# Kernel tuning notes

Measured on AMD Instinct MI355X. Metric: run time of the kernel, lower is better.

## Reference

```python
import jax, jax.numpy as jnp
import numpy as np

B, N, K = 8, 2048, 20  # clouds, points per cloud, knn


def _lin(k, i, o):
    kw, kb = jax.random.split(k)
    w = jax.random.normal(kw, (i, o), jnp.float32) / np.sqrt(i)
    b = jax.random.normal(kb, (o,), jnp.float32) * 0.01
    return w, b


def setup_inputs():
    key = jax.random.key(0)
    ks = jax.random.split(key, 9)
    pos = jax.random.normal(ks[0], (B * N, 3), jnp.float32)
    w11, b11 = _lin(ks[1], 3, 64)
    w12, b12 = _lin(ks[2], 64, 64)
    w13, b13 = _lin(ks[3], 64, 64)
    w21, b21 = _lin(ks[4], 192, 128)
    wh1, bh1 = _lin(ks[5], 128, 1024)
    wh2, bh2 = _lin(ks[6], 1024, 512)
    wh3, bh3 = _lin(ks[7], 512, 265)
    wh4, bh4 = _lin(ks[8], 265, 40)
    o, z = jnp.ones, jnp.zeros
    return dict(
        pos=pos,
        w11=w11, b11=b11, g11=o(64), be11=z(64),
        w12=w12, b12=b12, g12=o(64), be12=z(64),
        w13=w13, b13=b13, g13=o(64), be13=z(64),
        w21=w21, b21=b21, g21=o(128), be21=z(128),
        wh1=wh1, bh1=bh1, gh1=o(1024), beh1=z(1024),
        wh2=wh2, bh2=bh2, gh2=o(512), beh2=z(512),
        wh3=wh3, bh3=bh3, gh3=o(265), beh3=z(265),
        wh4=wh4, bh4=bh4,
    )


def _bn(x, g, b):
    # BatchNorm1d in training mode: stats over all leading dims, biased var.
    ax = tuple(range(x.ndim - 1))
    m = x.mean(ax)
    v = x.var(ax)
    return (x - m) * jax.lax.rsqrt(v + 1e-5) * g + b


def _forward(pos, w11, b11, g11, be11, w12, b12, g12, be12, w13, b13, g13, be13,
             w21, b21, g21, be21, wh1, bh1, gh1, beh1, wh2, bh2, gh2, beh2,
             wh3, bh3, gh3, beh3, wh4, bh4):
    p = pos.reshape(B, N, 3)
    # knn_graph per cloud, loop=False
    d2 = jnp.sum(p * p, -1)                                   # [B,N]
    dist = d2[:, :, None] + d2[:, None, :] - 2.0 * jnp.einsum('bnd,bmd->bnm', p, p)
    dist = dist + jnp.eye(N, dtype=pos.dtype) * 1e10          # exclude self
    _, idx = jax.lax.top_k(-dist, K)                          # [B,N,K]
    nb = jax.vmap(lambda a, i: a[i])(p, idx)                  # [B,N,K,3]
    rel = nb - p[:, :, None, :]                               # relative neighbor offsets
    # local PCA frame per point (V_t)
    cov = jnp.einsum('bnkd,bnke->bnde', rel, rel)             # [B,N,3,3]
    _, V = jnp.linalg.eigh(cov)                               # columns = principal dirs
    loc = jnp.einsum('bnkd,bnde->bnke', rel, V)               # rel pos in local frame
    # DD1: edge MLP (conv_p) + directional max pool (out_3d)
    h = _bn(jax.nn.relu(loc @ w11 + b11), g11, be11)
    h = _bn(jax.nn.relu(h @ w12 + b12), g12, be12)
    h = _bn(jax.nn.relu(h @ w13 + b13), g13, be13)            # [B,N,K,64]
    f3d = jnp.max(h[..., None] * loc[..., None, :], axis=2)   # [B,N,64,3]
    # DD2: gather neighbor 3d features (conv_fn), rotate into center frame, MLP, max pool
    fj = jax.vmap(lambda a, i: a[i])(f3d, idx)                # [B,N,K,64,3]
    fj_loc = jnp.einsum('bnkcd,bnde->bnkce', fj, V)
    h2 = _bn(jax.nn.relu(fj_loc.reshape(B, N, K, 192) @ w21 + b21), g21, be21)
    fdd2 = jnp.max(h2, axis=2).reshape(B * N, 128)
    # head
    y1 = (fdd2 @ wh1 + bh1).reshape(B, N, 1024).max(axis=1)
    y1 = _bn(jax.nn.relu(y1), gh1, beh1)
    y2 = _bn(jax.nn.relu(y1 @ wh2 + bh2), gh2, beh2)
    y3 = _bn(jax.nn.relu(y2 @ wh3 + bh3), gh3, beh3)
    return jax.nn.log_softmax(y3 @ wh4 + bh4, axis=1)         # [B,40]


def reference(pos, w11, b11, g11, be11, w12, b12, g12, be12, w13, b13, g13, be13,
              w21, b21, g21, be21, wh1, bh1, gh1, beh1, wh2, bh2, gh2, beh2,
              wh3, bh3, gh3, beh3, wh4, bh4):
    return _forward(pos, w11, b11, g11, be11, w12, b12, g12, be12, w13, b13, g13, be13,
                    w21, b21, g21, be21, wh1, bh1, gh1, beh1, wh2, bh2, gh2, beh2,
                    wh3, bh3, gh3, beh3, wh4, bh4)
```

## Files before the change

### kernel.cpp

```cpp
#include <hip/hip_runtime.h>


#define NEW_SLARTG 1

typedef unsigned short u16;
typedef unsigned int u32;
typedef unsigned long long u64;
typedef __attribute__((ext_vector_type(8))) short short8;
typedef __attribute__((ext_vector_type(4))) float f32x4;

#define BB 8
#define NNp 2048
#define KKn 20
#define NP 16384
#define EE 327680

__device__ __forceinline__ u32 fkey(float f) {
  u32 u = __float_as_uint(f);
  return (u & 0x80000000u) ? ~u : (u | 0x80000000u);
}
__device__ __forceinline__ float funkey(u32 k) {
  u32 u = (k & 0x80000000u) ? (k ^ 0x80000000u) : ~k;
  return __uint_as_float(u);
}
__device__ __forceinline__ float f_sign(float a, float b) {
  return (b >= 0.f) ? fabsf(a) : -fabsf(a);
}
__device__ __forceinline__ u16 f2bf(float f) {
  u32 u = __float_as_uint(f);
  u32 r = (u + 0x7fffu + ((u >> 16) & 1u)) >> 16;
  return (u16)r;
}

__device__ __forceinline__ u64 sxor64(u64 v, int m) {
  union { u64 q; u32 d[2]; } a; a.q = v;
  a.d[0] = __shfl_xor(a.d[0], m);
  a.d[1] = __shfl_xor(a.d[1], m);
  return a.q;
}
__device__ __forceinline__ u64 sidx64(u64 v, int src) {
  union { u64 q; u32 d[2]; } a; a.q = v;
  a.d[0] = __shfl(a.d[0], src);
  a.d[1] = __shfl(a.d[1], src);
  return a.q;
}
__device__ __forceinline__ void bsort64(u64& v, int lane) {
#pragma unroll
  for (int k = 2; k <= 64; k <<= 1) {
#pragma unroll
    for (int j = k >> 1; j > 0; j >>= 1) {
      u64 pv = sxor64(v, j);
      bool up = ((lane & k) == 0);
      bool lower = ((lane & j) == 0);
      bool keepmin = (lower == up);
      bool take = keepmin ? (pv < v) : (pv > v);
      v = take ? pv : v;
    }
  }
}

__device__ float slapy2_(float x, float y) {
#pragma clang fp contract(off)
  float xa = fabsf(x), ya = fabsf(y);
  float w = fmaxf(xa, ya), z = fminf(xa, ya);
  if (z == 0.f) return w;
  float t = z / w;
  return w * sqrtf(1.0f + t * t);
}

__device__ void slartg_(float f, float g, float& c, float& s, float& r) {
#pragma clang fp contract(off)
#if NEW_SLARTG
  const float safmin = 1.17549435e-38f;
  const float safmax = 8.50705917e+37f;
  const float rtmin = 1.08420217e-19f;
  const float rtmax = 6.52221171e+18f;
  float f1 = fabsf(f), g1 = fabsf(g);
  if (g == 0.f) { c = 1.f; s = 0.f; r = f; }
  else if (f == 0.f) { c = 0.f; s = (g >= 0.f) ? 1.f : -1.f; r = g1; }
  else {
    float d;
    if (f1 > rtmin && f1 < rtmax && g1 > rtmin && g1 < rtmax) {
      d = sqrtf(f * f + g * g);
      c = f1 / d;
      r = (f >= 0.f) ? d : -d;
    } else {
      float uu = fminf(safmax, fmaxf(safmin, fmaxf(f1, g1)));
      float fs = f / uu, gs = g / uu;
      d = sqrtf(fs * fs + gs * gs);
      c = fabsf(fs) / d;
      r = ((f >= 0.f) ? d : -d) * uu;
    }
    s = g / r;
  }
#else
  if (g == 0.f) { c = 1.f; s = 0.f; r = f; }
  else if (f == 0.f) { c = 0.f; s = 1.f; r = g; }
  else {
    float f1 = f, g1 = g;
    r = sqrtf(f1 * f1 + g1 * g1);
    c = f1 / r;
    s = g1 / r;
    if (fabsf(f) > fabsf(g) && c < 0.f) { c = -c; s = -s; r = -r; }
  }
#endif
}

__device__ void slaev2_(float a, float b, float c, float& rt1, float& rt2,
                        float& cs1, float& sn1) {
#pragma clang fp contract(off)
  float sm = a + c;
  float df = a - c;
  float adf = fabsf(df);
  float tb = b + b;
  float ab = fabsf(tb);
  float acmx, acmn;
  if (fabsf(a) > fabsf(c)) { acmx = a; acmn = c; } else { acmx = c; acmn = a; }
  float rt;
  if (adf > ab) { float t = ab / adf; rt = adf * sqrtf(1.f + t * t); }
  else if (adf < ab) { float t = adf / ab; rt = ab * sqrtf(1.f + t * t); }
  else { rt = ab * sqrtf(2.f); }
  int sgn1;
  if (sm < 0.f) {
    rt1 = 0.5f * (sm - rt); sgn1 = -1;
    rt2 = (acmx / rt1) * acmn - (b / rt1) * b;
  } else if (sm > 0.f) {
    rt1 = 0.5f * (sm + rt); sgn1 = 1;
    rt2 = (acmx / rt1) * acmn - (b / rt1) * b;
  } else {
    rt1 = 0.5f * rt; rt2 = -0.5f * rt; sgn1 = 1;
  }
  float cs; int sgn2;
  if (df >= 0.f) { cs = df + rt; sgn2 = 1; } else { cs = df - rt; sgn2 = -1; }
  float acs = fabsf(cs);
  if (acs > ab) {
    float ct = -tb / cs;
    sn1 = 1.f / sqrtf(1.f + ct * ct);
    cs1 = ct * sn1;
  } else {
    if (ab == 0.f) { cs1 = 1.f; sn1 = 0.f; }
    else {
      float tn = -cs / tb;
      cs1 = 1.f / sqrtf(1.f + tn * tn);
      sn1 = tn * cs1;
    }
  }
  if (sgn1 == sgn2) { float tn = cs1; cs1 = -sn1; sn1 = tn; }
}

__device__ void ssteqr3_(float* d, float* e, float z[3][3]) {
#pragma clang fp contract(off)
  const float eps = 5.9604645e-08f;
  const float eps2 = 3.5527137e-15f;
  const float safmin = 1.17549435e-38f;
  const int n = 3;
  const int nmaxit = 90;
  int jtot = 0;
  int l1 = 1;

  while (1) {
    if (l1 > n) break;
    if (l1 > 1) e[l1 - 2] = 0.f;
    int m = n;
    if (l1 <= n - 1) {
      for (int mm = l1; mm <= n - 1; ++mm) {
        float tst = fabsf(e[mm - 1]);
        if (tst == 0.f) { m = mm; break; }
        if (tst <= (sqrtf(fabsf(d[mm - 1])) * sqrtf(fabsf(d[mm]))) * eps) {
          e[mm - 1] = 0.f; m = mm; break;
        }
      }
    }
    int l = l1, lsv = l, lend = m, lendsv = lend;
    (void)lsv; (void)lendsv;
    l1 = m + 1;
    if (lend == l) continue;

    float anorm = 0.f;
    for (int i = l; i <= lend; ++i) anorm = fmaxf(anorm, fabsf(d[i - 1]));
    for (int i = l; i <= lend - 1; ++i) anorm = fmaxf(anorm, fabsf(e[i - 1]));
    if (anorm == 0.f) continue;

    if (fabsf(d[lend - 1]) < fabsf(d[l - 1])) { lend = lsv; l = lendsv; }

    if (lend > l) {
      while (1) {
        int m2 = lend;
        if (l != lend) {
          for (int mm = l; mm <= lend - 1; ++mm) {
            float tst = fabsf(e[mm - 1]); tst = tst * tst;
            if (tst <= (eps2 * fabsf(d[mm - 1])) * fabsf(d[mm]) + safmin) { m2 = mm; break; }
          }
        }
        if (m2 < lend) e[m2 - 1] = 0.f;
        float p = d[l - 1];
        if (m2 == l) {
          d[l - 1] = p; l += 1;
          if (l <= lend) continue;
          break;
        }
        if (m2 == l + 1) {
          float rt1, rt2, cc, ss;
          slaev2_(d[l - 1], e[l - 1], d[l], rt1, rt2, cc, ss);
          for (int i = 0; i < 3; ++i) {
            float temp = z[i][l];
            z[i][l] = cc * temp - ss * z[i][l - 1];
            z[i][l - 1] = ss * temp + cc * z[i][l - 1];
          }
          d[l - 1] = rt1; d[l] = rt2; e[l - 1] = 0.f;
          l += 2;
          if (l <= lend) continue;
          break;
        }
        if (jtot == nmaxit) break;
        jtot++;
        float g = (d[l] - p) / (2.f * e[l - 1]);
        float r = slapy2_(g, 1.f);
        g = d[m2 - 1] - p + (e[l - 1] / (g + f_sign(r, g)));
        float s = 1.f, c = 1.f;
        p = 0.f;
        float csv[2], snv[2];
        for (int i = m2 - 1; i >= l; --i) {
          float f = s * e[i - 1];
          float b = c * e[i - 1];
          slartg_(g, f, c, s, r);
          if (i != m2 - 1) e[i] = r;
          g = d[i] - p;
          r = (d[i - 1] - g) * s + (2.f * c) * b;
          p = s * r;
          d[i] = g + p;
          g = c * r - b;
          csv[i - l] = c; snv[i - l] = -s;
        }
        int cnt = m2 - l;
        for (int j = cnt; j >= 1; --j) {
          float cj = csv[j - 1], sj = snv[j - 1];
          int c0 = (l - 1) + (j - 1);
          for (int i = 0; i < 3; ++i) {
            float temp = z[i][c0 + 1];
            z[i][c0 + 1] = cj * temp - sj * z[i][c0];
            z[i][c0] = sj * temp + cj * z[i][c0];
          }
        }
        d[l - 1] = d[l - 1] - p;
        e[l - 1] = g;
      }
    } else {
      while (1) {
        int m2 = lend;
        if (l != lend) {
          for (int mm = l; mm >= lend + 1; --mm) {
            float tst = fabsf(e[mm - 2]); tst = tst * tst;
            if (tst <= (eps2 * fabsf(d[mm - 1])) * fabsf(d[mm - 2]) + safmin) { m2 = mm; break; }
          }
        }
        if (m2 > lend) e[m2 - 2] = 0.f;
        float p = d[l - 1];
        if (m2 == l) {
          d[l - 1] = p; l -= 1;
          if (l >= lend) continue;
          break;
        }
        if (m2 == l - 1) {
          float rt1, rt2, cc, ss;
          slaev2_(d[l - 2], e[l - 2], d[l - 1], rt1, rt2, cc, ss);
          for (int i = 0; i < 3; ++i) {
            float temp = z[i][l - 1];
            z[i][l - 1] = cc * temp - ss * z[i][l - 2];
            z[i][l - 2] = ss * temp + cc * z[i][l - 2];
          }
          d[l - 2] = rt1; d[l - 1] = rt2; e[l - 2] = 0.f;
          l -= 2;
          if (l >= lend) continue;
          break;
        }
        if (jtot == nmaxit) break;
        jtot++;
        float g = (d[l - 2] - p) / (2.f * e[l - 2]);
        float r = slapy2_(g, 1.f);
        g = d[m2 - 1] - p + (e[l - 2] / (g + f_sign(r, g)));
        float s = 1.f, c = 1.f;
        p = 0.f;
        float csv[2], snv[2];
        for (int i = m2; i <= l - 1; ++i) {
          float f = s * e[i - 1];
          float b = c * e[i - 1];
          slartg_(g, f, c, s, r);
          if (i != m2) e[i - 2] = r;
          g = d[i - 1] - p;
          r = (d[i] - g) * s + (2.f * c) * b;
          p = s * r;
          d[i - 1] = g + p;
          g = c * r - b;
          csv[i - m2] = c; snv[i - m2] = s;
        }
        int cnt = l - m2;
        for (int j = 1; j <= cnt; ++j) {
          float cj = csv[j - 1], sj = snv[j - 1];
          int c0 = (m2 - 1) + (j - 1);
          for (int i = 0; i < 3; ++i) {
            float temp = z[i][c0 + 1];
            z[i][c0 + 1] = cj * temp - sj * z[i][c0];
            z[i][c0] = sj * temp + cj * z[i][c0];
          }
        }
        d[l - 1] = d[l - 1] - p;
        e[l - 2] = g;
      }
    }
  }

  for (int ii = 2; ii <= n; ++ii) {
    int i = ii - 1, k = i;
    float p = d[i - 1];
    for (int j = ii; j <= n; ++j)
      if (d[j - 1] < p) { k = j; p = d[j - 1]; }
    if (k != i) {
      d[k - 1] = d[i - 1]; d[i - 1] = p;
      for (int r2 = 0; r2 < 3; ++r2) {
        float t = z[r2][i - 1]; z[r2][i - 1] = z[r2][k - 1]; z[r2][k - 1] = t;
      }
    }
  }
}

__device__ void eigh3_(float a00, float a10, float a11, float a20, float a21,
                       float a22, float V[3][3]) {
#pragma clang fp contract(off)
  float d0, d1, d2, e0, e1, tau1 = 0.f, v2 = 0.f;
  {
    float alpha = a10;
    float xnorm = fabsf(a20);
    if (xnorm == 0.f) {
      tau1 = 0.f; v2 = 0.f;
      e0 = alpha; d0 = a00; d1 = a11; d2 = a22; e1 = a21;
    } else {
      float beta = -f_sign(slapy2_(alpha, xnorm), alpha);
      tau1 = (beta - alpha) / beta;
      float inv = 1.0f / (alpha - beta);
      v2 = a20 * inv;
      float y0 = tau1 * a11;
      float y1v = tau1 * a21;
      float temp2 = a21 * v2;
      y0 = y0 + tau1 * temp2;
      y1v = y1v + (tau1 * v2) * a22;
      float dotyv = y0 * 1.f + y1v * v2;
      float al = (-0.5f * tau1) * dotyv;
      float w0 = y0 + al * 1.f;
      float w1 = y1v + al * v2;
      a11 = (a11 + 1.f * (-w0)) + w0 * (-1.f);
      a21 = (a21 + v2 * (-w0)) + w1 * (-1.f);
      a22 = (a22 + v2 * (-w1)) + w1 * (-v2);
      e0 = beta; d0 = a00; d1 = a11; d2 = a22; e1 = a21;
    }
  }
  float dd[3] = { d0, d1, d2 };
  float ee[2] = { e0, e1 };
  float z[3][3] = { {1.f,0.f,0.f},{0.f,1.f,0.f},{0.f,0.f,1.f} };
  ssteqr3_(dd, ee, z);
  if (tau1 != 0.f) {
    for (int j = 0; j < 3; ++j) {
      float wj = z[1][j] * 1.f + z[2][j] * v2;
      float temp = -tau1 * wj;
      z[1][j] = z[1][j] + 1.f * temp;
      z[2][j] = z[2][j] + v2 * temp;
    }
  }
  for (int r = 0; r < 3; ++r)
    for (int cix = 0; cix < 3; ++cix)
      V[r][cix] = z[r][cix];
}


__global__ void zero_kernel(double* sb, int nd, u32* p2, int n2) {
  int t = blockIdx.x * blockDim.x + threadIdx.x;
  if (t < nd) sb[t] = 0.0;
  if (t < n2) p2[t] = 0u;
}

__global__ __launch_bounds__(256) void knn_kernel(const float* __restrict__ pos,
                                                  int* __restrict__ idx) {
#pragma clang fp contract(off)
  __shared__ u64 cke[4][128];
  int w = threadIdx.x >> 6;
  int lane = threadIdx.x & 63;
  int wid = blockIdx.x * 4 + w;
  int b = wid >> 11;
  int n = wid & 2047;
  const float* pc = pos + (size_t)b * NNp * 3;
  float qx = pc[n * 3 + 0], qy = pc[n * 3 + 1], qz = pc[n * 3 + 2];
  float d2n = (qx * qx + qy * qy) + qz * qz;

  u32 kreg[32];
  u32 mk = 0xFFFFFFFFu;
#pragma unroll
  for (int t = 0; t < 32; ++t) {
    int m = lane + 64 * t;
    float x = pc[m * 3 + 0], y = pc[m * 3 + 1], zc = pc[m * 3 + 2];
    float d2m = (x * x + y * y) + zc * zc;
    float dot = (qx * x + qy * y) + qz * zc;
    float dist = (d2n + d2m) - 2.0f * dot;
    u32 key = fkey(dist);
    if (m == n) key = 0xFFFFFFFFu;
    kreg[t] = key;
    mk = key < mk ? key : mk;
  }
#pragma unroll
  for (int off = 32; off; off >>= 1) {
    u32 o = __shfl_xor(mk, off);
    mk = o < mk ? o : mk;
  }

  u32 lo_b = mk - 1u, hi_b = 0xFFFFFFFEu;
  int c_hi = 2047;
  float tf = funkey(mk) * 7.368f;
  u32 T = fkey(tf);
  if (T < mk) T = mk;
  if (T > 0xFFFFFFFEu) T = 0xFFFFFFFEu;
  for (int it = 0; it < 48; ++it) {
    int cnt = 0;
#pragma unroll
    for (int t = 0; t < 32; ++t) cnt += (kreg[t] <= T) ? 1 : 0;
#pragma unroll
    for (int off = 32; off; off >>= 1) cnt += __shfl_xor(cnt, off);
    if (cnt >= 20) {
      hi_b = T; c_hi = cnt;
      if (cnt <= 128) break;
    } else {
      lo_b = T;
    }
    if (hi_b <= lo_b + 1u) break;
    u32 Tn;
    if (it < 12) {
      float tfc = funkey(T);
      int cc = cnt < 1 ? 1 : cnt;
      float guess = tfc * __builtin_exp2f(0.66667f * __builtin_log2f(45.0f / (float)cc));
      Tn = fkey(guess);
      if (!(Tn > lo_b && Tn < hi_b)) Tn = lo_b + ((hi_b - lo_b) >> 1);
    } else {
      Tn = lo_b + ((hi_b - lo_b) >> 1);
    }
    T = Tn;
  }

  u64* ck = cke[w];
  u32 base = 0;
#pragma unroll
  for (int t = 0; t < 32; ++t) {
    bool pass = kreg[t] <= hi_b;
    u64 ball = __ballot(pass);
    if (pass) {
      u32 posn = base + (u32)__popcll(ball & ((1ull << lane) - 1ull));
      if (posn < 128u)
        ck[posn] = ((u64)kreg[t] << 32) | (u32)(lane + 64 * t);
    }
    base += (u32)__popcll(ball);
  }
  if (base > 128u) {
    base = 0;
#pragma unroll
    for (int t = 0; t < 32; ++t) {
      bool pass = kreg[t] <= lo_b;
      u64 ball = __ballot(pass);
      if (pass) {
        u32 posn = base + (u32)__popcll(ball & ((1ull << lane) - 1ull));
        ck[posn] = ((u64)kreg[t] << 32) | (u32)(lane + 64 * t);
      }
      base += (u32)__popcll(ball);
    }
#pragma unroll
    for (int t = 0; t < 32; ++t) {
      bool pass = (kreg[t] > lo_b) && (kreg[t] <= hi_b);
      u64 ball = __ballot(pass);
      if (pass) {
        u32 posn = base + (u32)__popcll(ball & ((1ull << lane) - 1ull));
        if (posn < 128u)
          ck[posn] = ((u64)kreg[t] << 32) | (u32)(lane + 64 * t);
      }
      base += (u32)__popcll(ball);
    }
  }
  u32 ctot = base < 128u ? base : 128u;

  u64 e0 = (lane < (int)ctot) ? ck[lane] : ~0ull;
  bsort64(e0, lane);
  if (ctot > 64u) {
    u64 e1 = (lane + 64 < (int)ctot) ? ck[lane + 64] : ~0ull;
    bsort64(e1, lane);
    u64 r = sidx64(e1, 63 - lane);
    u64 mn = r < e0 ? r : e0;
#pragma unroll
    for (int j = 32; j > 0; j >>= 1) {
      u64 pv = sxor64(mn, j);
      bool lower2 = ((lane & j) == 0);
      bool take = lower2 ? (pv < mn) : (pv > mn);
      mn = take ? pv : mn;
    }
    e0 = mn;
  }
  if (lane < 20)
    idx[(size_t)wid * 20 + lane] = (int)(u32)(e0 & 0xFFFFFFFFull);
}

__global__ __launch_bounds__(64) void prep_kernel(const float* __restrict__ pos,
                                                  const int* __restrict__ idx,
                                                  float* __restrict__ loc,
                                                  float* __restrict__ Vout) {
#pragma clang fp contract(off)
  int p = blockIdx.x * 64 + threadIdx.x;
  int b = p >> 11, n = p & 2047;
  const float* pc = pos + (size_t)b * NNp * 3;
  float qx = pc[n * 3 + 0], qy = pc[n * 3 + 1], qz = pc[n * 3 + 2];
  const int* ip = idx + (size_t)p * 20;
  float c00 = 0, c01 = 0, c02 = 0, c11 = 0, c12 = 0, c22 = 0;
  for (int k = 0; k < 20; ++k) {
    int j = ip[k];
    float rx = pc[j * 3 + 0] - qx, ry = pc[j * 3 + 1] - qy, rz = pc[j * 3 + 2] - qz;
    c00 += rx * rx; c01 += rx * ry; c02 += rx * rz;
    c11 += ry * ry; c12 += ry * rz; c22 += rz * rz;
  }
  float Vm[3][3];
  eigh3_(c00, c01, c11, c02, c12, c22, Vm);
  float* vp = Vout + (size_t)p * 9;
  for (int d = 0; d < 3; ++d)
    for (int e = 0; e < 3; ++e) vp[d * 3 + e] = Vm[d][e];
  for (int k = 0; k < 20; ++k) {
    int j = ip[k];
    float rx = pc[j * 3 + 0] - qx, ry = pc[j * 3 + 1] - qy, rz = pc[j * 3 + 2] - qz;
    float l0 = rx * Vm[0][0] + ry * Vm[1][0] + rz * Vm[2][0];
    float l1 = rx * Vm[0][1] + ry * Vm[1][1] + rz * Vm[2][1];
    float l2 = rx * Vm[0][2] + ry * Vm[1][2] + rz * Vm[2][2];
    size_t e = ((size_t)p * 20 + k) * 3;
    loc[e + 0] = l0; loc[e + 1] = l1; loc[e + 2] = l2;
  }
}

__global__ __launch_bounds__(256) void l1_kernel(const float* __restrict__ loc,
                                                 const float* __restrict__ W,
                                                 const float* __restrict__ bias,
                                                 float* __restrict__ h1,
                                                 double* __restrict__ sb) {
  __shared__ float sW[192];
  __shared__ float sB[64];
  __shared__ float red[512];
  int t = threadIdx.x;
  if (t < 192) sW[t] = W[t];
  if (t < 64) sB[t] = bias[t];
  __syncthreads();
  int w = t >> 6, c = t & 63;
  size_t e0 = (size_t)blockIdx.x * 256 + w * 64;
  float wc0 = sW[c], wc1 = sW[64 + c], wc2 = sW[128 + c], bc = sB[c];
  float s = 0.f, q = 0.f;
  for (int e = 0; e < 64; ++e) {
    float x0 = loc[(e0 + e) * 3 + 0];
    float x1 = loc[(e0 + e) * 3 + 1];
    float x2 = loc[(e0 + e) * 3 + 2];
    float z = fmaxf(bc + x0 * wc0 + x1 * wc1 + x2 * wc2, 0.f);
    h1[(e0 + e) * 64 + c] = z;
    s += z; q += z * z;
  }
  red[w * 64 + c] = s;
  red[256 + w * 64 + c] = q;
  __syncthreads();
  if (t < 64) {
    float S = red[t] + red[64 + t] + red[128 + t] + red[192 + t];
    float Q = red[256 + t] + red[320 + t] + red[384 + t] + red[448 + t];
    atomicAdd(&sb[((int)blockIdx.x & 63) * 128 + t], (double)S);
    atomicAdd(&sb[((int)blockIdx.x & 63) * 128 + 64 + t], (double)Q);
  }
}

__global__ void finalizeB_kernel(const double* __restrict__ sb,
                                 const float* __restrict__ g,
                                 const float* __restrict__ be,
                                 float* __restrict__ outp) {
  int c = threadIdx.x;
  if (c >= 64) return;
  double s = 0.0, q = 0.0;
  for (int buk = 0; buk < 64; ++buk) {
    s += sb[buk * 128 + c];
    q += sb[buk * 128 + 64 + c];
  }
  double m = s / (double)EE;
  double var = q / (double)EE - m * m;
  double inv = 1.0 / sqrt(var + 1e-5);
  double sc = (double)g[c] * inv;
  outp[c] = (float)sc;
  outp[64 + c] = (float)((double)be[c] - m * sc);
}

__global__ void finalize64_kernel(const double* __restrict__ s4b,
                                  const float* __restrict__ g,
                                  const float* __restrict__ be,
                                  float* __restrict__ outp) {
  int c = threadIdx.x;
  double s = 0.0, q = 0.0;
  for (int buk = 0; buk < 64; ++buk) {
    s += s4b[buk * 256 + c];
    q += s4b[buk * 256 + 128 + c];
  }
  double m = s / (double)EE;
  double var = q / (double)EE - m * m;
  double inv = 1.0 / sqrt(var + 1e-5);
  double sc = (double)g[c] * inv;
  outp[c] = (float)sc;
  outp[128 + c] = (float)((double)be[c] - m * sc);
}

__global__ __launch_bounds__(256) void wsplit_kernel(const float* __restrict__ w12,
                                                     const float* __restrict__ w13,
                                                     u16* __restrict__ wsp) {
  int id = blockIdx.x * 256 + threadIdx.x;
  if (id >= 8192) return;
  int layer = id >> 12;
  int nk = id & 4095;
  int n = nk >> 6, k = nk & 63;
  const float* W = layer ? w13 : w12;
  float v = W[(size_t)k * 64 + n];
  u16 hi = f2bf(v);
  float rem = v - __uint_as_float(((u32)hi) << 16);
  u16 lo = f2bf(rem);
  wsp[layer * 8192 + n * 64 + k] = hi;
  wsp[layer * 8192 + 4096 + n * 64 + k] = lo;
}

__global__ __launch_bounds__(256) void l23_kernel(const float* __restrict__ hin,
                                                  const float* __restrict__ ss,
                                                  const u16* __restrict__ whi,
                                                  const u16* __restrict__ wlo,
                                                  const float* __restrict__ bias,
                                                  float* __restrict__ hout,
                                                  double* __restrict__ sb) {
  __shared__ u16 sHI[128 * 72];
  __shared__ u16 sLO[128 * 72];
  int t = threadIdx.x;
  size_t e0 = (size_t)blockIdx.x * 128;
  int w = t >> 6, l = t & 63;
  int lr = l & 15, lg = l >> 4;

  short8 bhi[4][2], blo[4][2];
#pragma unroll
  for (int nt = 0; nt < 4; ++nt)
#pragma unroll
    for (int ks = 0; ks < 2; ++ks) {
      int off = (nt * 16 + lr) * 64 + ks * 32 + lg * 8;
      bhi[nt][ks] = *(const short8*)&whi[off];
      blo[nt][ks] = *(const short8*)&wlo[off];
    }

  for (int v = t; v < 128 * 16; v += 256) {
    int el = v >> 4, cq = v & 15;
    float4 x4 = *(const float4*)&hin[(e0 + el) * 64 + cq * 4];
    float4 sc4 = *(const float4*)&ss[cq * 4];
    float4 sh4 = *(const float4*)&ss[64 + cq * 4];
    float vv[4];
    vv[0] = x4.x * sc4.x + sh4.x;
    vv[1] = x4.y * sc4.y + sh4.y;
    vv[2] = x4.z * sc4.z + sh4.z;
    vv[3] = x4.w * sc4.w + sh4.w;
    u16 hi[4], lo[4];
#pragma unroll
    for (int j = 0; j < 4; ++j) {
      hi[j] = f2bf(vv[j]);
      float rem = vv[j] - __uint_as_float(((u32)hi[j]) << 16);
      lo[j] = f2bf(rem);
    }
    u32* ph = (u32*)&sHI[el * 72 + cq * 4];
    ph[0] = (u32)hi[0] | ((u32)hi[1] << 16);
    ph[1] = (u32)hi[2] | ((u32)hi[3] << 16);
    u32* pl = (u32*)&sLO[el * 72 + cq * 4];
    pl[0] = (u32)lo[0] | ((u32)lo[1] << 16);
    pl[1] = (u32)lo[2] | ((u32)lo[3] << 16);
  }
  __syncthreads();

  f32x4 acc[2][4];
#pragma unroll
  for (int mt = 0; mt < 2; ++mt)
#pragma unroll
    for (int nt = 0; nt < 4; ++nt) acc[mt][nt] = (f32x4)(0.f);

#pragma unroll
  for (int ks = 0; ks < 2; ++ks) {
    const int kb = ks * 32 + lg * 8;
#pragma unroll
    for (int mt = 0; mt < 2; ++mt) {
      int row = w * 32 + mt * 16 + lr;
      short8 ah = *(const short8*)&sHI[row * 72 + kb];
      short8 al = *(const short8*)&sLO[row * 72 + kb];
#pragma unroll
      for (int nt = 0; nt < 4; ++nt) {
        acc[mt][nt] = __builtin_amdgcn_mfma_f32_16x16x32_bf16(ah, bhi[nt][ks], acc[mt][nt], 0, 0, 0);
        acc[mt][nt] = __builtin_amdgcn_mfma_f32_16x16x32_bf16(al, bhi[nt][ks], acc[mt][nt], 0, 0, 0);
        acc[mt][nt] = __builtin_amdgcn_mfma_f32_16x16x32_bf16(ah, blo[nt][ks], acc[mt][nt], 0, 0, 0);
      }
    }
  }

#pragma unroll
  for (int nt = 0; nt < 4; ++nt) {
    int o = nt * 16 + lr;
    float bs = bias[o];
    float s = 0.f, q = 0.f;
#pragma unroll
    for (int mt = 0; mt < 2; ++mt) {
#pragma unroll
      for (int r = 0; r < 4; ++r) {
        float z = fmaxf(acc[mt][nt][r] + bs, 0.f);
        size_t e = e0 + w * 32 + mt * 16 + lg * 4 + r;
        hout[e * 64 + o] = z;
        s += z; q += z * z;
      }
    }
    s += __shfl_xor(s, 16); s += __shfl_xor(s, 32);
    q += __shfl_xor(q, 16); q += __shfl_xor(q, 32);
    if (l < 16) {
      atomicAdd(&sb[((int)blockIdx.x & 63) * 128 + o], (double)s);
      atomicAdd(&sb[((int)blockIdx.x & 63) * 128 + 64 + o], (double)q);
    }
  }
}

__global__ __launch_bounds__(256) void f3d_kernel(const float* __restrict__ h3,
                                                  const float* __restrict__ ss3,
                                                  const float* __restrict__ loc,
                                                  float* __restrict__ f3d) {
  int t = threadIdx.x;
  int p = blockIdx.x * 4 + (t >> 6);
  int c = t & 63;
  float sc = ss3[c], sh = ss3[64 + c];
  float m0 = -__builtin_inff(), m1 = m0, m2 = m0;
  size_t eb = (size_t)p * 20;
  for (int k = 0; k < 20; ++k) {
    size_t e = eb + k;
    float h = h3[e * 64 + c] * sc + sh;
    float l0 = loc[e * 3 + 0], l1 = loc[e * 3 + 1], l2 = loc[e * 3 + 2];
    m0 = fmaxf(m0, h * l0);
    m1 = fmaxf(m1, h * l1);
    m2 = fmaxf(m2, h * l2);
  }
  size_t o = (size_t)p * 192 + c * 3;
  f3d[o + 0] = m0; f3d[o + 1] = m1; f3d[o + 2] = m2;
}

__global__ __launch_bounds__(256) void wtcvt_kernel(const float* __restrict__ W,
                                                    u16* __restrict__ wt,
                                                    double* __restrict__ s4b) {
  int id = blockIdx.x * 256 + threadIdx.x;
  if (id < 192 * 128) {
    int n = id / 192, k = id - n * 192;
    wt[id] = f2bf(W[(size_t)k * 128 + n]);
  }
  if (id < 64 * 256) s4b[id] = 0.0;
}

__global__ __launch_bounds__(256) void dd2_kernel(const float* __restrict__ f3d,
                                                  const float* __restrict__ Vmat,
                                                  const int* __restrict__ idx,
                                                  const u16* __restrict__ wt,
                                                  const float* __restrict__ bias,
                                                  float* __restrict__ fdd2T,
                                                  double* __restrict__ s4b) {
  __shared__ u16 sX[80 * 200];
  __shared__ float sV[36];
  __shared__ int sJ[80];
  int t = threadIdx.x;
  int wk = (blockIdx.x & 7) * 512 + (blockIdx.x >> 3);
  int p0 = wk * 4;
  int bcl = p0 >> 11;
  int buk = ((int)blockIdx.x & 63) << 8;

  int w = t >> 6, l = t & 63;
  int lr = l & 15, lg = l >> 4;

  short8 breg[2][6];
#pragma unroll
  for (int nt = 0; nt < 2; ++nt)
#pragma unroll
    for (int s = 0; s < 6; ++s) {
      const int kk = (s / 3) * 96 + (s % 3) * 32 + lg * 8;
      breg[nt][s] = *(const short8*)&wt[(w * 32 + nt * 16 + lr) * 192 + kk];
    }

  if (t < 36) sV[t] = Vmat[(size_t)p0 * 9 + t];
  if (t < 80) sJ[t] = ((bcl << 11) + idx[(size_t)p0 * 20 + t]) * 192;
  __syncthreads();

  for (int v = t; v < 80 * 32; v += 256) {
    int el = v >> 5, c2 = v & 31;
    int pp = el / 20;
    const float* fp = f3d + (size_t)sJ[el] + 6 * c2;
    float f0 = fp[0], f1 = fp[1], f2 = fp[2];
    float f3 = fp[3], f4 = fp[4], f5 = fp[5];
    const float* Vp = &sV[pp * 9];
    float x0 = f0 * Vp[0] + f1 * Vp[3] + f2 * Vp[6];
    float x1 = f0 * Vp[1] + f1 * Vp[4] + f2 * Vp[7];
    float x2 = f0 * Vp[2] + f1 * Vp[5] + f2 * Vp[8];
    float y0 = f3 * Vp[0] + f4 * Vp[3] + f5 * Vp[6];
    float y1 = f3 * Vp[1] + f4 * Vp[4] + f5 * Vp[7];
    float y2 = f3 * Vp[2] + f4 * Vp[5] + f5 * Vp[8];
    u32* xp = (u32*)&sX[el * 200 + 6 * c2];
    xp[0] = (u32)f2bf(x0) | ((u32)f2bf(x1) << 16);
    xp[1] = (u32)f2bf(x2) | ((u32)f2bf(y0) << 16);
    xp[2] = (u32)f2bf(y1) | ((u32)f2bf(y2) << 16);
  }
  __syncthreads();

  f32x4 acc[5][2];
#pragma unroll
  for (int mt = 0; mt < 5; ++mt) {
    acc[mt][0] = (f32x4)(0.f);
    acc[mt][1] = (f32x4)(0.f);
  }

#pragma unroll
  for (int s = 0; s < 6; ++s) {
    const int kbase = (s / 3) * 96 + (s % 3) * 32 + lg * 8;
#pragma unroll
    for (int mt = 0; mt < 5; ++mt) {
      short8 a = *(const short8*)&sX[(mt * 16 + lr) * 200 + kbase];
      acc[mt][0] = __builtin_amdgcn_mfma_f32_16x16x32_bf16(a, breg[0][s], acc[mt][0], 0, 0, 0);
      acc[mt][1] = __builtin_amdgcn_mfma_f32_16x16x32_bf16(a, breg[1][s], acc[mt][1], 0, 0, 0);
    }
  }

#pragma unroll
  for (int nt = 0; nt < 2; ++nt) {
    int col = w * 32 + nt * 16 + lr;
    float bs = bias[col];
    float pm0 = 0.f, pm1 = 0.f, pm2 = 0.f, pm3 = 0.f;
    float s = 0.f, q = 0.f;
#pragma unroll
    for (int mt = 0; mt < 5; ++mt) {
#pragma unroll
      for (int r = 0; r < 4; ++r) {
        int edge = mt * 16 + lg * 4 + r;
        float z = fmaxf(acc[mt][nt][r] + bs, 0.f);
        pm0 = fmaxf(pm0, (edge < 20) ? z : 0.f);
        pm1 = fmaxf(pm1, (edge >= 20 && edge < 40) ? z : 0.f);
        pm2 = fmaxf(pm2, (edge >= 40 && edge < 60) ? z : 0.f);
        pm3 = fmaxf(pm3, (edge >= 60) ? z : 0.f);
        s += z; q += z * z;
      }
    }
#pragma unroll
    for (int off = 16; off < 64; off <<= 1) {
      pm0 = fmaxf(pm0, __shfl_xor(pm0, off));
      pm1 = fmaxf(pm1, __shfl_xor(pm1, off));
      pm2 = fmaxf(pm2, __shfl_xor(pm2, off));
      pm3 = fmaxf(pm3, __shfl_xor(pm3, off));
      s += __shfl_xor(s, off);
      q += __shfl_xor(q, off);
    }
    if (l < 16) {
      float4 pv;
      pv.x = pm0; pv.y = pm1; pv.z = pm2; pv.w = pm3;
      *(float4*)&fdd2T[(size_t)col * NP + p0] = pv;
      atomicAdd(&s4b[buk + col], (double)s);
      atomicAdd(&s4b[buk + 128 + col], (double)q);
    }
  }
}

__global__ __launch_bounds__(256) void y1_kernel(const float* __restrict__ fdd2T,
                                                 const float* __restrict__ ss4,
                                                 const float* __restrict__ wh1,
                                                 u32* __restrict__ y1key) {
  __shared__ float sX[64][128];
  __shared__ float sW[64][128];
  int t = threadIdx.x;
  int mtile = blockIdx.x & 127;
  int ntile = blockIdx.x >> 7;
  int cl = mtile >> 4;
  size_t pbase = (size_t)mtile * 128;
  int c0 = ntile * 128;
  int mg = t >> 4, ng = t & 15;

  float acc[8][8];
#pragma unroll
  for (int i = 0; i < 8; ++i)
#pragma unroll
    for (int j = 0; j < 8; ++j) acc[i][j] = 0.f;

  for (int ks = 0; ks < 2; ++ks) {
    int rr = t >> 5, mq = t & 31;
#pragma unroll
    for (int i = 0; i < 8; ++i) {
      int r = rr + i * 8;
      int k = ks * 64 + r;
      float4 x4 = *(const float4*)&fdd2T[(size_t)k * NP + pbase + mq * 4];
      float sc = ss4[k], sh = ss4[128 + k];
      float4 st;
      st.x = x4.x * sc + sh;
      st.y = x4.y * sc + sh;
      st.z = x4.z * sc + sh;
      st.w = x4.w * sc + sh;
      *(float4*)&sX[r][mq * 4] = st;
      float4 w4 = *(const float4*)&wh1[(size_t)k * 1024 + c0 + mq * 4];
      *(float4*)&sW[r][mq * 4] = w4;
    }
    __syncthreads();
#pragma unroll 8
    for (int kk = 0; kk < 64; ++kk) {
      float4 xa = *(const float4*)&sX[kk][mg * 4];
      float4 xb = *(const float4*)&sX[kk][64 + mg * 4];
      float4 wa = *(const float4*)&sW[kk][ng * 4];
      float4 wb = *(const float4*)&sW[kk][64 + ng * 4];
      float xr[8] = { xa.x, xa.y, xa.z, xa.w, xb.x, xb.y, xb.z, xb.w };
      float wc[8] = { wa.x, wa.y, wa.z, wa.w, wb.x, wb.y, wb.z, wb.w };
#pragma unroll
      for (int i = 0; i < 8; ++i)
#pragma unroll
        for (int j = 0; j < 8; ++j) acc[i][j] += xr[i] * wc[j];
    }
    __syncthreads();
  }

  float colmax[8];
#pragma unroll
  for (int j = 0; j < 8; ++j) {
    float v = acc[0][j];
#pragma unroll
    for (int i = 1; i < 8; ++i) v = fmaxf(v, acc[i][j]);
    colmax[j] = v;
  }
  float* red = &sX[0][0];
#pragma unroll
  for (int j = 0; j < 8; ++j) {
    int col = (j < 4) ? (ng * 4 + j) : (64 + ng * 4 + (j - 4));
    red[col * 16 + mg] = colmax[j];
  }
  __syncthreads();
  if (t < 128) {
    float m = red[t * 16];
#pragma unroll
    for (int i = 1; i < 16; ++i) m = fmaxf(m, red[t * 16 + i]);
    atomicMax(&y1key[(size_t)cl * 1024 + c0 + t], fkey(m));
  }
}

__global__ void y1bn_kernel(const u32* __restrict__ y1key,
                            const float* __restrict__ bh1,
                            const float* __restrict__ g,
                            const float* __restrict__ be,
                            float* __restrict__ y1n) {
  int c = blockIdx.x * 256 + threadIdx.x;
  if (c >= 1024) return;
  float bs = bh1[c];
  float v[8]; double s = 0.0;
#pragma unroll
  for (int b = 0; b < 8; ++b) {
    v[b] = fmaxf(funkey(y1key[b * 1024 + c]) + bs, 0.f);
    s += (double)v[b];
  }
  double m = s / 8.0, q = 0.0;
#pragma unroll
  for (int b = 0; b < 8; ++b) { double d = (double)v[b] - m; q += d * d; }
  q /= 8.0;
  double inv = 1.0 / sqrt(q + 1e-5);
  double sg = (double)g[c] * inv;
#pragma unroll
  for (int b = 0; b < 8; ++b)
    y1n[b * 1024 + c] = (float)(((double)v[b] - m) * sg + (double)be[c]);
}

__global__ __launch_bounds__(256) void hgemm_kernel(const float* __restrict__ yin,
                                                    const float* __restrict__ W,
                                                    float* __restrict__ part,
                                                    int INn, int OUTn, int notile) {
  __shared__ float sx[8 * 128];
  __shared__ float red[4][8][64];
  int t = threadIdx.x;
  int og = blockIdx.x % notile;
  int ks = blockIdx.x / notile;
  int KC = INn >> 3;
  int k0 = ks * KC;
  for (int v = t; v < 8 * KC; v += 256) {
    int b = v / KC, i = v - b * KC;
    sx[b * KC + i] = yin[(size_t)b * INn + k0 + i];
  }
  __syncthreads();
  int o = og * 64 + (t & 63);
  int kq = t >> 6;
  int sub = KC >> 2;
  float acc[8];
#pragma unroll
  for (int b = 0; b < 8; ++b) acc[b] = 0.f;
  if (o < OUTn) {
    for (int i = kq * sub; i < kq * sub + sub; ++i) {
      float w = W[(size_t)(k0 + i) * OUTn + o];
#pragma unroll
      for (int b = 0; b < 8; ++b) acc[b] += sx[b * KC + i] * w;
    }
  }
#pragma unroll
  for (int b = 0; b < 8; ++b) red[kq][b][t & 63] = acc[b];
  __syncthreads();
  if (kq == 0 && o < OUTn) {
#pragma unroll
    for (int b = 0; b < 8; ++b) {
      float s = ((red[0][b][t] + red[1][b][t]) + red[2][b][t]) + red[3][b][t];
      part[(size_t)(ks * 8 + b) * 512 + o] = s;
    }
  }
}

__global__ void hreduce_kernel(const float* __restrict__ part,
                               const float* __restrict__ bias,
                               const float* __restrict__ g,
                               const float* __restrict__ be,
                               float* __restrict__ yout, int OUTn) {
  int o = blockIdx.x * 256 + threadIdx.x;
  if (o >= OUTn) return;
  float bs = bias[o];
  float v[8]; double s = 0.0;
#pragma unroll
  for (int b = 0; b < 8; ++b) {
    float p = 0.f;
#pragma unroll
    for (int ks = 0; ks < 8; ++ks) p += part[(size_t)(ks * 8 + b) * 512 + o];
    v[b] = fmaxf(p + bs, 0.f);
    s += (double)v[b];
  }
  double m = s / 8.0, q = 0.0;
#pragma unroll
  for (int b = 0; b < 8; ++b) { double d = (double)v[b] - m; q += d * d; }
  q /= 8.0;
  double inv = 1.0 / sqrt(q + 1e-5);
  double sg = (double)g[o] * inv;
#pragma unroll
  for (int b = 0; b < 8; ++b)
    yout[(size_t)b * OUTn + o] = (float)(((double)v[b] - m) * sg + (double)be[o]);
}

__global__ __launch_bounds__(384) void logits_kernel(const float* __restrict__ y3n,
                                                     const float* __restrict__ W,
                                                     const float* __restrict__ bias,
                                                     float* __restrict__ out) {
  __shared__ float sy[8 * 265];
  __shared__ float slog[320];
  __shared__ float sm[8], sl[8];
  int t = threadIdx.x;
  for (int v = t; v < 8 * 265; v += 384) sy[v] = y3n[v];
  __syncthreads();
  if (t < 320) {
    int b = t / 40, o = t % 40;
    float acc = 0.f;
    for (int i = 0; i < 265; ++i) acc += sy[b * 265 + i] * W[i * 40 + o];
    slog[t] = acc + bias[o];
  }
  __syncthreads();
  if (t < 8) {
    float m = slog[t * 40];
    for (int o = 1; o < 40; ++o) m = fmaxf(m, slog[t * 40 + o]);
    float s = 0.f;
    for (int o = 0; o < 40; ++o) s += expf(slog[t * 40 + o] - m);
    sm[t] = m; sl[t] = logf(s);
  }
  __syncthreads();
  if (t < 320) {
    int b = t / 40;
    out[t] = slog[t] - sm[b] - sl[b];
  }
}

extern "C" void kernel_launch(void* const* d_in, const int* in_sizes, int n_in,
                              void* d_out, int out_size, void* d_ws, size_t ws_size,
                              hipStream_t stream) {
  (void)in_sizes; (void)n_in; (void)out_size; (void)ws_size;
  const float* pos  = (const float*)d_in[0];
  const float* w11  = (const float*)d_in[1];
  const float* b11  = (const float*)d_in[2];
  const float* g11  = (const float*)d_in[3];
  const float* be11 = (const float*)d_in[4];
  const float* w12  = (const float*)d_in[5];
  const float* b12  = (const float*)d_in[6];
  const float* g12  = (const float*)d_in[7];
  const float* be12 = (const float*)d_in[8];
  const float* w13  = (const float*)d_in[9];
  const float* b13  = (const float*)d_in[10];
  const float* g13  = (const float*)d_in[11];
  const float* be13 = (const float*)d_in[12];
  const float* w21  = (const float*)d_in[13];
  const float* b21  = (const float*)d_in[14];
  const float* g21  = (const float*)d_in[15];
  const float* be21 = (const float*)d_in[16];
  const float* wh1  = (const float*)d_in[17];
  const float* bh1  = (const float*)d_in[18];
  const float* gh1  = (const float*)d_in[19];
  const float* beh1 = (const float*)d_in[20];
  const float* wh2  = (const float*)d_in[21];
  const float* bh2  = (const float*)d_in[22];
  const float* gh2  = (const float*)d_in[23];
  const float* beh2 = (const float*)d_in[24];
  const float* wh3  = (const float*)d_in[25];
  const float* bh3  = (const float*)d_in[26];
  const float* gh3  = (const float*)d_in[27];
  const float* beh3 = (const float*)d_in[28];
  const float* wh4  = (const float*)d_in[29];
  const float* bh4  = (const float*)d_in[30];

  char* ws = (char*)d_ws;
  int*    idx   = (int*)(ws + 0);
  float*  loc   = (float*)(ws + 1310720);
  float*  V     = (float*)(ws + 5242880);
  float*  h     = (float*)(ws + 5832704);
  u16*    wt    = (u16*)(ws + 5832704);
  double* s4b   = (double*)(ws + 5898240);
  float*  hpart = (float*)(ws + 6881280);
  float*  f3d   = (float*)(ws + 89718784);
  double* sbkt  = (double*)(ws + 89718784);
  u16*    wsp   = (u16*)(ws + 89718784 + 196608);
  float*  fdd2T = (float*)(ws + 102301696);
  u32*    y1k   = (u32*)(ws + 110690304);
  float*  y1n   = (float*)(ws + 110723072);
  float*  y2n   = (float*)(ws + 110755840);
  float*  y3n   = (float*)(ws + 110772224);
  float*  param = (float*)(ws + 110785856);
  float*  out   = (float*)d_out;

  double* sbL1 = sbkt;
  double* sbL2 = sbkt + 8192;
  double* sbL3 = sbkt + 16384;

  zero_kernel<<<96, 256, 0, stream>>>(sbkt, 24576, y1k, 8192);
  wsplit_kernel<<<32, 256, 0, stream>>>(w12, w13, wsp);
  knn_kernel<<<4096, 256, 0, stream>>>(pos, idx);
  prep_kernel<<<256, 64, 0, stream>>>(pos, idx, loc, V);

  l1_kernel<<<1280, 256, 0, stream>>>(loc, w11, b11, h, sbL1);
  finalizeB_kernel<<<1, 64, 0, stream>>>(sbL1, g11, be11, param);

  l23_kernel<<<2560, 256, 0, stream>>>(h, param, wsp, wsp + 4096, b12, h, sbL2);
  finalizeB_kernel<<<1, 64, 0, stream>>>(sbL2, g12, be12, param + 128);

  l23_kernel<<<2560, 256, 0, stream>>>(h, param + 128, wsp + 8192, wsp + 12288, b13, h, sbL3);
  finalizeB_kernel<<<1, 64, 0, stream>>>(sbL3, g13, be13, param + 256);

  f3d_kernel<<<4096, 256, 0, stream>>>(h, param + 256, loc, f3d);
  wtcvt_kernel<<<96, 256, 0, stream>>>(w21, wt, s4b);
  dd2_kernel<<<4096, 256, 0, stream>>>(f3d, V, idx, wt, b21, fdd2T, s4b);
  finalize64_kernel<<<1, 128, 0, stream>>>(s4b, g21, be21, param + 384);

  y1_kernel<<<1024, 256, 0, stream>>>(fdd2T, param + 384, wh1, y1k);
  y1bn_kernel<<<4, 256, 0, stream>>>(y1k, bh1, gh1, beh1, y1n);

  hgemm_kernel<<<64, 256, 0, stream>>>(y1n, wh2, hpart, 1024, 512, 8);
  hreduce_kernel<<<2, 256, 0, stream>>>(hpart, bh2, gh2, beh2, y2n, 512);
  hgemm_kernel<<<40, 256, 0, stream>>>(y2n, wh3, hpart, 512, 265, 5);
  hreduce_kernel<<<2, 256, 0, stream>>>(hpart, bh3, gh3, beh3, y3n, 265);
  logits_kernel<<<1, 384, 0, stream>>>(y3n, wh4, bh4, out);
}
```

Measured before the change: 370.0 us.

## Fuse head BN/reduce into GEMMs, merge init kernels, tweak dd2 and y1 tiling

Merges the zero and weight-split kernels into one init kernel. The head's BN and partial-sum reduction kernels are folded into the following GEMM and logits kernels, cutting five small launches; each block now recomputes the BN for its slice. dd2 uses float2 gathers and a per-quad max in its epilogue, and y1 halves its shared-memory K tile, which lowers LDS use but doubles the number of sync steps.

```diff
diff --git a/kernel.cpp b/kernel.cpp
--- a/kernel.cpp
+++ b/kernel.cpp
@@ -372,10 +372,26 @@
 }
 
 
-__global__ void zero_kernel(double* sb, int nd, u32* p2, int n2) {
-  int t = blockIdx.x * blockDim.x + threadIdx.x;
-  if (t < nd) sb[t] = 0.0;
-  if (t < n2) p2[t] = 0u;
+__global__ __launch_bounds__(256) void init_kernel(double* __restrict__ sb,
+                                                   u32* __restrict__ y1k,
+                                                   const float* __restrict__ w12,
+                                                   const float* __restrict__ w13,
+                                                   u16* __restrict__ wsp) {
+  int id = blockIdx.x * 256 + threadIdx.x;
+  if (id < 24576) sb[id] = 0.0;
+  if (id < 8192) {
+    y1k[id] = 0u;
+    int layer = id >> 12;
+    int nk = id & 4095;
+    int n = nk >> 6, k = nk & 63;
+    const float* W = layer ? w13 : w12;
+    float v = W[(size_t)k * 64 + n];
+    u16 hi = f2bf(v);
+    float rem = v - __uint_as_float(((u32)hi) << 16);
+    u16 lo = f2bf(rem);
+    wsp[layer * 8192 + n * 64 + k] = hi;
+    wsp[layer * 8192 + 4096 + n * 64 + k] = lo;
+  }
 }
 
 __global__ __launch_bounds__(256) void knn_kernel(const float* __restrict__ pos,
@@ -605,23 +621,6 @@
   double sc = (double)g[c] * inv;
   outp[c] = (float)sc;
   outp[128 + c] = (float)((double)be[c] - m * sc);
-}
-
-__global__ __launch_bounds__(256) void wsplit_kernel(const float* __restrict__ w12,
-                                                     const float* __restrict__ w13,
-                                                     u16* __restrict__ wsp) {
-  int id = blockIdx.x * 256 + threadIdx.x;
-  if (id >= 8192) return;
-  int layer = id >> 12;
-  int nk = id & 4095;
-  int n = nk >> 6, k = nk & 63;
-  const float* W = layer ? w13 : w12;
-  float v = W[(size_t)k * 64 + n];
-  u16 hi = f2bf(v);
-  float rem = v - __uint_as_float(((u32)hi) << 16);
-  u16 lo = f2bf(rem);
-  wsp[layer * 8192 + n * 64 + k] = hi;
-  wsp[layer * 8192 + 4096 + n * 64 + k] = lo;
 }
 
 __global__ __launch_bounds__(256) void l23_kernel(const float* __restrict__ hin,
@@ -790,8 +789,11 @@
     int el = v >> 5, c2 = v & 31;
     int pp = el / 20;
     const float* fp = f3d + (size_t)sJ[el] + 6 * c2;
-    float f0 = fp[0], f1 = fp[1], f2 = fp[2];
-    float f3 = fp[3], f4 = fp[4], f5 = fp[5];
+    float2 f01 = *(const float2*)(fp);
+    float2 f23 = *(const float2*)(fp + 2);
+    float2 f45 = *(const float2*)(fp + 4);
+    float f0 = f01.x, f1 = f01.y, f2 = f23.x;
+    float f3 = f23.y, f4 = f45.x, f5 = f45.y;
     const float* Vp = &sV[pp * 9];
     float x0 = f0 * Vp[0] + f1 * Vp[3] + f2 * Vp[6];
     float x1 = f0 * Vp[1] + f1 * Vp[4] + f2 * Vp[7];
@@ -832,16 +834,21 @@
     float s = 0.f, q = 0.f;
 #pragma unroll
     for (int mt = 0; mt < 5; ++mt) {
-#pragma unroll
-      for (int r = 0; r < 4; ++r) {
-        int edge = mt * 16 + lg * 4 + r;
-        float z = fmaxf(acc[mt][nt][r] + bs, 0.f);
-        pm0 = fmaxf(pm0, (edge < 20) ? z : 0.f);
-        pm1 = fmaxf(pm1, (edge >= 20 && edge < 40) ? z : 0.f);
-        pm2 = fmaxf(pm2, (edge >= 40 && edge < 60) ? z : 0.f);
-        pm3 = fmaxf(pm3, (edge >= 60) ? z : 0.f);
-        s += z; q += z * z;
-      }
+      int qs = mt * 16 + lg * 4;
+      int qp = qs / 20;
+      float z0 = fmaxf(acc[mt][nt][0] + bs, 0.f);
+      float z1 = fmaxf(acc[mt][nt][1] + bs, 0.f);
+      float z2 = fmaxf(acc[mt][nt][2] + bs, 0.f);
+      float z3 = fmaxf(acc[mt][nt][3] + bs, 0.f);
+      s += z0; q += z0 * z0;
+      s += z1; q += z1 * z1;
+      s += z2; q += z2 * z2;
+      s += z3; q += z3 * z3;
+      float qm = fmaxf(fmaxf(z0, z1), fmaxf(z2, z3));
+      pm0 = fmaxf(pm0, (qp == 0) ? qm : 0.f);
+      pm1 = fmaxf(pm1, (qp == 1) ? qm : 0.f);
+      pm2 = fmaxf(pm2, (qp == 2) ? qm : 0.f);
+      pm3 = fmaxf(pm3, (qp == 3) ? qm : 0.f);
     }
 #pragma unroll
     for (int off = 16; off < 64; off <<= 1) {
@@ -866,8 +873,8 @@
                                                  const float* __restrict__ ss4,
                                                  const float* __restrict__ wh1,
                                                  u32* __restrict__ y1key) {
-  __shared__ float sX[64][128];
-  __shared__ float sW[64][128];
+  __shared__ float sX[32][128];
+  __shared__ float sW[32][128];
   int t = threadIdx.x;
   int mtile = blockIdx.x & 127;
   int ntile = blockIdx.x >> 7;
@@ -882,12 +889,12 @@
 #pragma unroll
     for (int j = 0; j < 8; ++j) acc[i][j] = 0.f;
 
-  for (int ks = 0; ks < 2; ++ks) {
+  for (int ks = 0; ks < 4; ++ks) {
     int rr = t >> 5, mq = t & 31;
 #pragma unroll
-    for (int i = 0; i < 8; ++i) {
+    for (int i = 0; i < 4; ++i) {
       int r = rr + i * 8;
-      int k = ks * 64 + r;
+      int k = ks * 32 + r;
       float4 x4 = *(const float4*)&fdd2T[(size_t)k * NP + pbase + mq * 4];
       float sc = ss4[k], sh = ss4[128 + k];
       float4 st;
@@ -901,7 +908,7 @@
     }
     __syncthreads();
 #pragma unroll 8
-    for (int kk = 0; kk < 64; ++kk) {
+    for (int kk = 0; kk < 32; ++kk) {
       float4 xa = *(const float4*)&sX[kk][mg * 4];
       float4 xb = *(const float4*)&sX[kk][64 + mg * 4];
       float4 wa = *(const float4*)&sW[kk][ng * 4];
@@ -939,64 +946,52 @@
   }
 }
 
-__global__ void y1bn_kernel(const u32* __restrict__ y1key,
-                            const float* __restrict__ bh1,
-                            const float* __restrict__ g,
-                            const float* __restrict__ be,
-                            float* __restrict__ y1n) {
-  int c = blockIdx.x * 256 + threadIdx.x;
-  if (c >= 1024) return;
-  float bs = bh1[c];
-  float v[8]; double s = 0.0;
-#pragma unroll
-  for (int b = 0; b < 8; ++b) {
-    v[b] = fmaxf(funkey(y1key[b * 1024 + c]) + bs, 0.f);
-    s += (double)v[b];
-  }
-  double m = s / 8.0, q = 0.0;
-#pragma unroll
-  for (int b = 0; b < 8; ++b) { double d = (double)v[b] - m; q += d * d; }
-  q /= 8.0;
-  double inv = 1.0 / sqrt(q + 1e-5);
-  double sg = (double)g[c] * inv;
-#pragma unroll
-  for (int b = 0; b < 8; ++b)
-    y1n[b * 1024 + c] = (float)(((double)v[b] - m) * sg + (double)be[c]);
-}
-
-__global__ __launch_bounds__(256) void hgemm_kernel(const float* __restrict__ yin,
-                                                    const float* __restrict__ W,
-                                                    float* __restrict__ part,
-                                                    int INn, int OUTn, int notile) {
+__global__ __launch_bounds__(256) void hgemm1_kernel(const u32* __restrict__ y1k,
+                                                     const float* __restrict__ bh1,
+                                                     const float* __restrict__ gh1,
+                                                     const float* __restrict__ beh1,
+                                                     const float* __restrict__ W,
+                                                     float* __restrict__ part) {
   __shared__ float sx[8 * 128];
   __shared__ float red[4][8][64];
   int t = threadIdx.x;
-  int og = blockIdx.x % notile;
-  int ks = blockIdx.x / notile;
-  int KC = INn >> 3;
-  int k0 = ks * KC;
-  for (int v = t; v < 8 * KC; v += 256) {
-    int b = v / KC, i = v - b * KC;
-    sx[b * KC + i] = yin[(size_t)b * INn + k0 + i];
+  int og = blockIdx.x & 7;
+  int ks = blockIdx.x >> 3;
+  int k0 = ks * 128;
+  if (t < 128) {
+    int c = k0 + t;
+    float bs = bh1[c];
+    float v[8]; double s = 0.0;
+#pragma unroll
+    for (int b = 0; b < 8; ++b) {
+      v[b] = fmaxf(funkey(y1k[b * 1024 + c]) + bs, 0.f);
+      s += (double)v[b];
+    }
+    double m = s / 8.0, q = 0.0;
+#pragma unroll
+    for (int b = 0; b < 8; ++b) { double d = (double)v[b] - m; q += d * d; }
+    q /= 8.0;
+    double inv = 1.0 / sqrt(q + 1e-5);
+    double sg = (double)gh1[c] * inv;
+#pragma unroll
+    for (int b = 0; b < 8; ++b)
+      sx[b * 128 + t] = (float)(((double)v[b] - m) * sg + (double)beh1[c]);
   }
   __syncthreads();
   int o = og * 64 + (t & 63);
   int kq = t >> 6;
-  int sub = KC >> 2;
   float acc[8];
 #pragma unroll
   for (int b = 0; b < 8; ++b) acc[b] = 0.f;
-  if (o < OUTn) {
-    for (int i = kq * sub; i < kq * sub + sub; ++i) {
-      float w = W[(size_t)(k0 + i) * OUTn + o];
-#pragma unroll
-      for (int b = 0; b < 8; ++b) acc[b] += sx[b * KC + i] * w;
-    }
+  for (int i = kq * 32; i < kq * 32 + 32; ++i) {
+    float w = W[(size_t)(k0 + i) * 512 + o];
+#pragma unroll
+    for (int b = 0; b < 8; ++b) acc[b] += sx[b * 128 + i] * w;
   }
 #pragma unroll
   for (int b = 0; b < 8; ++b) red[kq][b][t & 63] = acc[b];
   __syncthreads();
-  if (kq == 0 && o < OUTn) {
+  if (kq == 0) {
 #pragma unroll
     for (int b = 0; b < 8; ++b) {
       float s = ((red[0][b][t] + red[1][b][t]) + red[2][b][t]) + red[3][b][t];
@@ -1005,35 +1000,69 @@
   }
 }
 
-__global__ void hreduce_kernel(const float* __restrict__ part,
-                               const float* __restrict__ bias,
-                               const float* __restrict__ g,
-                               const float* __restrict__ be,
-                               float* __restrict__ yout, int OUTn) {
-  int o = blockIdx.x * 256 + threadIdx.x;
-  if (o >= OUTn) return;
-  float bs = bias[o];
-  float v[8]; double s = 0.0;
-#pragma unroll
-  for (int b = 0; b < 8; ++b) {
-    float p = 0.f;
-#pragma unroll
-    for (int ks = 0; ks < 8; ++ks) p += part[(size_t)(ks * 8 + b) * 512 + o];
-    v[b] = fmaxf(p + bs, 0.f);
-    s += (double)v[b];
-  }
-  double m = s / 8.0, q = 0.0;
-#pragma unroll
-  for (int b = 0; b < 8; ++b) { double d = (double)v[b] - m; q += d * d; }
-  q /= 8.0;
-  double inv = 1.0 / sqrt(q + 1e-5);
-  double sg = (double)g[o] * inv;
-#pragma unroll
-  for (int b = 0; b < 8; ++b)
-    yout[(size_t)b * OUTn + o] = (float)(((double)v[b] - m) * sg + (double)be[o]);
-}
-
-__global__ __launch_bounds__(384) void logits_kernel(const float* __restrict__ y3n,
+__global__ __launch_bounds__(256) void hgemm2_kernel(const float* __restrict__ part,
+                                                     const float* __restrict__ bh2,
+                                                     const float* __restrict__ gh2,
+                                                     const float* __restrict__ beh2,
+                                                     const float* __restrict__ W,
+                                                     float* __restrict__ part2) {
+  __shared__ float sx[8 * 64];
+  __shared__ float red[4][8][64];
+  int t = threadIdx.x;
+  int og = blockIdx.x % 5;
+  int ks = blockIdx.x / 5;
+  int k0 = ks * 64;
+  if (t < 64) {
+    int c = k0 + t;
+    float bs = bh2[c];
+    float v[8]; double s = 0.0;
+#pragma unroll
+    for (int b = 0; b < 8; ++b) {
+      float p = 0.f;
+#pragma unroll
+      for (int c2 = 0; c2 < 8; ++c2) p += part[(size_t)(c2 * 8 + b) * 512 + c];
+      v[b] = fmaxf(p + bs, 0.f);
+      s += (double)v[b];
+    }
+    double m = s / 8.0, q = 0.0;
+#pragma unroll
+    for (int b = 0; b < 8; ++b) { double d = (double)v[b] - m; q += d * d; }
+    q /= 8.0;
+    double inv = 1.0 / sqrt(q + 1e-5);
+    double sg = (double)gh2[c] * inv;
+#pragma unroll
+    for (int b = 0; b < 8; ++b)
+      sx[b * 64 + t] = (float)(((double)v[b] - m) * sg + (double)beh2[c]);
+  }
+  __syncthreads();
+  int o = og * 64 + (t & 63);
+  int kq = t >> 6;
+  float acc[8];
+#pragma unroll
+  for (int b = 0; b < 8; ++b) acc[b] = 0.f;
+  if (o < 265) {
+    for (int i = kq * 16; i < kq * 16 + 16; ++i) {
+      float w = W[(size_t)(k0 + i) * 265 + o];
+#pragma unroll
+      for (int b = 0; b < 8; ++b) acc[b] += sx[b * 64 + i] * w;
+    }
+  }
+#pragma unroll
+  for (int b = 0; b < 8; ++b) red[kq][b][t & 63] = acc[b];
+  __syncthreads();
+  if (kq == 0 && o < 265) {
+#pragma unroll
+    for (int b = 0; b < 8; ++b) {
+      float s = ((red[0][b][t] + red[1][b][t]) + red[2][b][t]) + red[3][b][t];
+      part2[(size_t)(ks * 8 + b) * 512 + o] = s;
+    }
+  }
+}
+
+__global__ __launch_bounds__(384) void logits_kernel(const float* __restrict__ part2,
+                                                     const float* __restrict__ bh3,
+                                                     const float* __restrict__ gh3,
+                                                     const float* __restrict__ beh3,
                                                      const float* __restrict__ W,
                                                      const float* __restrict__ bias,
                                                      float* __restrict__ out) {
@@ -1041,7 +1070,27 @@
   __shared__ float slog[320];
   __shared__ float sm[8], sl[8];
   int t = threadIdx.x;
-  for (int v = t; v < 8 * 265; v += 384) sy[v] = y3n[v];
+  if (t < 265) {
+    float bs = bh3[t];
+    float v[8]; double s = 0.0;
+#pragma unroll
+    for (int b = 0; b < 8; ++b) {
+      float p = 0.f;
+#pragma unroll
+      for (int c2 = 0; c2 < 8; ++c2) p += part2[(size_t)(c2 * 8 + b) * 512 + t];
+      v[b] = fmaxf(p + bs, 0.f);
+      s += (double)v[b];
+    }
+    double m = s / 8.0, q = 0.0;
+#pragma unroll
+    for (int b = 0; b < 8; ++b) { double d = (double)v[b] - m; q += d * d; }
+    q /= 8.0;
+    double inv = 1.0 / sqrt(q + 1e-5);
+    double sg = (double)gh3[t] * inv;
+#pragma unroll
+    for (int b = 0; b < 8; ++b)
+      sy[b * 265 + t] = (float)(((double)v[b] - m) * sg + (double)beh3[t]);
+  }
   __syncthreads();
   if (t < 320) {
     int b = t / 40, o = t % 40;
@@ -1108,14 +1157,12 @@
   u16*    wt    = (u16*)(ws + 5832704);
   double* s4b   = (double*)(ws + 5898240);
   float*  hpart = (float*)(ws + 6881280);
+  float*  hpart2= (float*)(ws + 7012352);
   float*  f3d   = (float*)(ws + 89718784);
   double* sbkt  = (double*)(ws + 89718784);
   u16*    wsp   = (u16*)(ws + 89718784 + 196608);
   float*  fdd2T = (float*)(ws + 102301696);
   u32*    y1k   = (u32*)(ws + 110690304);
-  float*  y1n   = (float*)(ws + 110723072);
-  float*  y2n   = (float*)(ws + 110755840);
-  float*  y3n   = (float*)(ws + 110772224);
   float*  param = (float*)(ws + 110785856);
   float*  out   = (float*)d_out;
 
@@ -1123,8 +1170,7 @@
   double* sbL2 = sbkt + 8192;
   double* sbL3 = sbkt + 16384;
 
-  zero_kernel<<<96, 256, 0, stream>>>(sbkt, 24576, y1k, 8192);
-  wsplit_kernel<<<32, 256, 0, stream>>>(w12, w13, wsp);
+  init_kernel<<<96, 256, 0, stream>>>(sbkt, y1k, w12, w13, wsp);
   knn_kernel<<<4096, 256, 0, stream>>>(pos, idx);
   prep_kernel<<<256, 64, 0, stream>>>(pos, idx, loc, V);
 
@@ -1143,11 +1189,8 @@
   finalize64_kernel<<<1, 128, 0, stream>>>(s4b, g21, be21, param + 384);
 
   y1_kernel<<<1024, 256, 0, stream>>>(fdd2T, param + 384, wh1, y1k);
-  y1bn_kernel<<<4, 256, 0, stream>>>(y1k, bh1, gh1, beh1, y1n);
-
-  hgemm_kernel<<<64, 256, 0, stream>>>(y1n, wh2, hpart, 1024, 512, 8);
-  hreduce_kernel<<<2, 256, 0, stream>>>(hpart, bh2, gh2, beh2, y2n, 512);
-  hgemm_kernel<<<40, 256, 0, stream>>>(y2n, wh3, hpart, 512, 265, 5);
-  hreduce_kernel<<<2, 256, 0, stream>>>(hpart, bh3, gh3, beh3, y3n, 265);
-  logits_kernel<<<1, 384, 0, stream>>>(y3n, wh4, bh4, out);
-}
+
+  hgemm1_kernel<<<64, 256, 0, stream>>>(y1k, bh1, gh1, beh1, wh2, hpart);
+  hgemm2_kernel<<<40, 256, 0, stream>>>(hpart, bh2, gh2, beh2, wh3, hpart2);
+  logits_kernel<<<1, 384, 0, stream>>>(hpart2, bh3, gh3, beh3, wh4, bh4, out);
+}
```

Result: faster. 352.3 us (-4.8%).
